# Kernel tuning notes

Hardware: AMD Instinct MI355X
Metric: run time of the kernel (lower is better)

The kernel has to match this reference:

```python
import jax, jax.numpy as jnp
import numpy as np

PAD = 0
EPS = 1e-5


def setup_inputs() -> dict:
    key = jax.random.key(0)
    k1, k2, k3, k4, k5 = jax.random.split(key, 5)
    B, S, D, H = 16, 1024, 512, 4
    output = jax.random.normal(k1, (B, S, D), dtype=jnp.float32)
    local_cor = jax.random.normal(k2, (1,), dtype=jnp.float32)
    event_type = jax.random.randint(k3, (B, S), 0, 1000, dtype=jnp.int64)
    # xavier-ish scale for the per-layer Linear weights
    W = jax.random.normal(k4, (H, D, D), dtype=jnp.float32) * (1.0 / np.sqrt(D))
    b = jax.random.normal(k5, (H, D), dtype=jnp.float32) * 0.01
    return {"output": output, "local_cor": local_cor, "event_type": event_type, "W": W, "b": b}


def _build_mask(event_type, S, dtype):
    # subsequent mask: 1 for strictly-future positions (triu, diag=1)
    subseq = jnp.triu(jnp.ones((S, S), dtype=dtype), k=1)  # [S,S]
    # key-pad mask: 1 where key token is PAD, broadcast over query dim
    keypad = (event_type == PAD).astype(dtype)[:, None, :]  # [B,1,S]
    return ((keypad + subseq[None]) > 0).astype(dtype)  # [B,S,S]


def reference(output, local_cor, event_type, W, b):
    B, S, D = output.shape
    H = W.shape[0]
    temperature = jnp.asarray(D, output.dtype) ** 0.5
    mask = _build_mask(event_type, S, output.dtype)  # [B,S,S]

    x = output
    total = None
    for h in range(H):  # heads are applied SEQUENTIALLY in the original
        # masked QK^T scores
        attn = jnp.einsum('bqd,bkd->bqk', x / temperature, x) * mask  # [B,S,S]
        # L2 normalize along keys (F.normalize p=2, eps=1e-5)
        norm = jnp.sqrt(jnp.sum(attn * attn, axis=-1, keepdims=True))
        attn = attn / jnp.maximum(norm, EPS)
        # value path: ELU(Linear(x))
        v = jax.nn.elu(jnp.einsum('bsd,ed->bse', x, W[h]) + b[h])  # [B,S,D]
        x = jnp.einsum('bqk,bkd->bqd', attn, v)
        total = x if total is None else total + x
    return total
```

## Files before the change

kernel.cpp:

```cpp
#include <hip/hip_runtime.h>
#include <math.h>

#define B_ 16
#define S_ 1024
#define D_ 512
#define H_ 4
#define INV_TEMP 0.044194173824159216f
#define C_SCALE 0.00390625f
#define OUT_SCALE 256.0f

typedef _Float16 f16;
typedef _Float16 f16x8 __attribute__((ext_vector_type(8)));
typedef _Float16 f16x4 __attribute__((ext_vector_type(4)));
typedef float f32x4 __attribute__((ext_vector_type(4)));

#define AS1(p) ((const __attribute__((address_space(1))) void*)(p))
#define AS3(p) ((__attribute__((address_space(3))) void*)(p))
#define MFMA __builtin_amdgcn_mfma_f32_16x16x32_f16

#define SBAR()                                                                 \
    do {                                                                       \
        __builtin_amdgcn_sched_barrier(0);                                     \
        __builtin_amdgcn_s_barrier();                                          \
        __builtin_amdgcn_sched_barrier(0);                                     \
    } while (0)
#define VMF(N)                                                                 \
    do {                                                                       \
        __builtin_amdgcn_sched_barrier(0);                                     \
        asm volatile("s_waitcnt vmcnt(" #N ")" ::: "memory");                  \
        __builtin_amdgcn_sched_barrier(0);                                     \
    } while (0)

__device__ __forceinline__ f16x8 ds_rd16(unsigned addr)
{
    f16x8 r;
    asm volatile("ds_read_b128 %0, %1" : "=v"(r) : "v"(addr));
    return r;
}

__global__ __launch_bounds__(256)
void k_pre(const float* __restrict__ x0, f16* __restrict__ xh,
           const float* __restrict__ W, f16* __restrict__ Wh,
           const int* __restrict__ etype, int* __restrict__ flag,
           float* __restrict__ ssb)
{
    const int t = threadIdx.x;
    const int bi = blockIdx.x;
    if (bi < 8192) {
        const int xcd = bi & 7, j = bi >> 3;
        const int b = 2 * xcd + (j & 1);
        const int off = j >> 1;
        const int i = (b * 512 + off) * 256 + t;
        const float4 v = ((const float4*)x0)[i];
        f16x4 h; h[0] = (f16)v.x; h[1] = (f16)v.y; h[2] = (f16)v.z; h[3] = (f16)v.w;
        ((f16x4*)xh)[i] = h;
    } else if (bi < 9216) {
        const int i = (bi - 8192) * 256 + t;
        const float4 v = ((const float4*)W)[i];
        f16x4 h; h[0] = (f16)v.x; h[1] = (f16)v.y; h[2] = (f16)v.z; h[3] = (f16)v.w;
        ((f16x4*)Wh)[i] = h;
    } else if (bi == 9216) {
        if (t < 128) {
            const int b = t >> 3, kt = t & 7;
            const int* p = etype + b * S_ + kt * 128;
            int any0 = 0;
#pragma unroll
            for (int i = 0; i < 128; i += 4) {
                const int4 v = *(const int4*)(p + i);
                any0 |= (v.x == 0) | (v.y == 0) | (v.z == 0) | (v.w == 0);
            }
            flag[t] = any0;
        }
    } else {
        const int i = (bi - 9217) * 256 + t;
        ((float4*)ssb)[i] = make_float4(0.f, 0.f, 0.f, 0.f);
    }
}

__device__ __forceinline__ void stage128x64(const f16* __restrict__ src, int ld,
                                            char* lds0, int t)
{
    const int r = t >> 3;
    const int c = ((t & 7) ^ (r & 7)) << 3;
    const f16* g = src + (size_t)r * ld + c;
#pragma unroll
    for (int j = 0; j < 4; ++j)
        __builtin_amdgcn_global_load_lds(AS1(g + (size_t)(32 * j) * ld),
                                         AS3(lds0 + j * 4096 + t * 16), 16, 0, 0);
}

__device__ __forceinline__ void mma_asm(unsigned aB, unsigned bB,
                                        const unsigned (*offA)[2],
                                        const unsigned (*offB)[2],
                                        f32x4 (*acc)[4])
{
    f16x8 af[4][2], bf[4][2];
#pragma unroll
    for (int kk = 0; kk < 2; ++kk) {
#pragma unroll
        for (int i = 0; i < 4; ++i) af[i][kk] = ds_rd16(aB + offA[i][kk]);
#pragma unroll
        for (int j = 0; j < 4; ++j) bf[j][kk] = ds_rd16(bB + offB[j][kk]);
    }
    asm volatile("s_waitcnt lgkmcnt(0)" ::: "memory");
    __builtin_amdgcn_sched_barrier(0);
#pragma unroll
    for (int kk = 0; kk < 2; ++kk)
#pragma unroll
        for (int i = 0; i < 4; ++i)
#pragma unroll
            for (int j = 0; j < 4; ++j)
                acc[i][j] = MFMA(af[i][kk], bf[j][kk], acc[i][j], 0, 0, 0);
}

__device__ __forceinline__ void gemm_cnt(const f16* __restrict__ A, int ldA,
                                         const f16* __restrict__ Bm, int ldB,
                                         char* lds, int t,
                                         const unsigned (*offA)[2],
                                         const unsigned (*offB)[2],
                                         f32x4 (*acc)[4])
{
    const unsigned base = (unsigned)(unsigned long long)AS3(lds);
    stage128x64(A, ldA, lds, t);
    stage128x64(Bm, ldB, lds + 16384, t);
#pragma unroll 1
    for (int i = 0; i < 3; ++i) {
        const int k1 = i * 128 + 64, k2 = i * 128 + 128;
        stage128x64(A + k1, ldA, lds + 32768, t);
        stage128x64(Bm + k1, ldB, lds + 49152, t);
        VMF(8); SBAR();
        mma_asm(base, base + 16384, offA, offB, acc);
        SBAR();
        stage128x64(A + k2, ldA, lds, t);
        stage128x64(Bm + k2, ldB, lds + 16384, t);
        VMF(8); SBAR();
        mma_asm(base + 32768, base + 49152, offA, offB, acc);
        SBAR();
    }
    stage128x64(A + 448, ldA, lds + 32768, t);
    stage128x64(Bm + 448, ldB, lds + 49152, t);
    VMF(8); SBAR();
    mma_asm(base, base + 16384, offA, offB, acc);
    SBAR();
    VMF(0); SBAR();
    mma_asm(base + 32768, base + 49152, offA, offB, acc);
}

__global__ __launch_bounds__(256)
void k_vs(const f16* __restrict__ xh, const f16* __restrict__ Wh,
          const float* __restrict__ bias, f16* __restrict__ vT,
          const int* __restrict__ etype, const int* __restrict__ flag,
          f16* __restrict__ sh, float* __restrict__ ss)
{
    __shared__ __align__(16) char lds[65536];
    const int t = threadIdx.x;
    const int w = t >> 6, lane = t & 63, lr = lane & 15, quad = lane >> 4;
    const int wm = w & 1, wn = w >> 1;

    unsigned offA[4][2], offB[4][2];
#pragma unroll
    for (int i = 0; i < 4; ++i) {
        const int ra = wm * 64 + i * 16 + lr;
        const int rb = wn * 64 + i * 16 + lr;
#pragma unroll
        for (int kk = 0; kk < 2; ++kk) {
            offA[i][kk] = (unsigned)((ra << 7) + ((((kk << 2) + quad) ^ (ra & 7)) << 4));
            offB[i][kk] = (unsigned)((rb << 7) + ((((kk << 2) + quad) ^ (rb & 7)) << 4));
        }
    }

    if (blockIdx.x < 1024) {
        const int i0 = blockIdx.x;
        const int xcd = i0 & 7, j0 = i0 >> 3;
        const int b = 2 * xcd + (j0 & 1);
        const int tile = j0 >> 1;
        const int bk = (tile & 7) * 128;
        const int bq = (tile >> 3) * 128;
        if (bk < bq && !flag[b * 8 + (bk >> 7)]) return;

        const f16* xb = xh + (size_t)b * S_ * D_;
        f32x4 acc[4][4] = {};
        gemm_cnt(xb + (size_t)bk * D_, D_, xb + (size_t)bq * D_, D_,
                 lds, t, offA, offB, acc);
        const float sc = INV_TEMP * C_SCALE;
        float ssq[4] = {0.0f, 0.0f, 0.0f, 0.0f};
#pragma unroll
        for (int i = 0; i < 4; ++i) {
            const int k4 = bk + wm * 64 + i * 16 + quad * 4;
            const int4 et = *(const int4*)(etype + b * S_ + k4);
            const int ev[4] = {et.x, et.y, et.z, et.w};
#pragma unroll
            for (int j = 0; j < 4; ++j) {
                const int q = bq + wn * 64 + j * 16 + lr;
                f16x4 hv;
#pragma unroll
                for (int r = 0; r < 4; ++r) {
                    const bool keep = ((k4 + r) > q) || (ev[r] == 0);
                    hv[r] = (f16)(keep ? acc[i][j][r] * sc : 0.0f);
                    const float fv = (float)hv[r];
                    ssq[j] += fv * fv;
                }
                *(f16x4*)(sh + ((size_t)b * S_ + q) * S_ + k4) = hv;
            }
        }
#pragma unroll
        for (int j = 0; j < 4; ++j) {
            float v = ssq[j];
            v += __shfl_xor(v, 16, 64);
            v += __shfl_xor(v, 32, 64);
            if (quad == 0) {
                const int q = bq + wn * 64 + j * 16 + lr;
                atomicAdd(ss + b * S_ + q, v);
            }
        }
    } else {
        const int idx = blockIdx.x - 1024;
        const int xcd = idx & 7;
        const int b = 2 * xcd + ((idx >> 3) & 1);
        const int rest = idx >> 4;
        const int sq = rest & 7;
        const int bn = (rest >> 3) * 128;
        const int bm = b * 1024 + sq * 128;
        f32x4 acc[4][4] = {};
        gemm_cnt(xh + (size_t)bm * D_, D_, Wh + (size_t)bn * D_, D_,
                 lds, t, offA, offB, acc);
#pragma unroll
        for (int j = 0; j < 4; ++j) {
            const int e = bn + wn * 64 + j * 16 + lr;
            const float be = bias[e];
#pragma unroll
            for (int i = 0; i < 4; ++i) {
                const int s = sq * 128 + wm * 64 + i * 16 + quad * 4;
                f16x4 hv;
#pragma unroll
                for (int r = 0; r < 4; ++r) {
                    float z = acc[i][j][r] + be;
                    z = (z > 0.0f) ? z : (expf(z) - 1.0f);
                    hv[r] = (f16)z;
                }
                *(f16x4*)(vT + ((size_t)b * D_ + e) * S_ + s) = hv;
            }
        }
    }
}

__device__ __forceinline__ void mma64(const char* ldsA, const char* ldsB,
                                      int wm, int wn, int lr, int quad,
                                      f32x4 (*acc)[4])
{
#pragma unroll
    for (int kk = 0; kk < 2; ++kk) {
        f16x8 af[4], bf[4];
#pragma unroll
        for (int i = 0; i < 4; ++i) {
            const int row = wm * 64 + i * 16 + lr;
            af[i] = *(const f16x8*)(ldsA + (row << 7) +
                                    ((((kk << 2) + quad) ^ (row & 7)) << 4));
        }
#pragma unroll
        for (int j = 0; j < 4; ++j) {
            const int row = wn * 64 + j * 16 + lr;
            bf[j] = *(const f16x8*)(ldsB + (row << 7) +
                                    ((((kk << 2) + quad) ^ (row & 7)) << 4));
        }
#pragma unroll
        for (int i = 0; i < 4; ++i)
#pragma unroll
            for (int j = 0; j < 4; ++j)
                acc[i][j] = MFMA(af[i], bf[j], acc[i][j], 0, 0, 0);
    }
}

__global__ __launch_bounds__(512)
void k_out(const f16* __restrict__ vT, const f16* __restrict__ sh,
           const float* __restrict__ ss, const int* __restrict__ flag,
           f16* __restrict__ xh_w,
           const f16* __restrict__ xs0, const f16* __restrict__ xs1,
           const f16* __restrict__ xs2,
           float* __restrict__ out, const int accum, const int wout)
{
    __shared__ __align__(16) char lds[65536];
    __shared__ int klist[32];
    __shared__ int kcnt;
    const int t = threadIdx.x;
    const int g = t >> 8;
    const int tl = t & 255;
    const int w = tl >> 6, lane = tl & 63, lr = lane & 15, quad = lane >> 4;
    const int wm = w & 1, wn = w >> 1;
    const int i0 = blockIdx.x;
    const int xcd = i0 & 7, j0 = i0 >> 3;
    const int b = 2 * xcd + (j0 & 1);
    const int tile = j0 >> 1;
    const int be = (tile & 3) * 128;
    const int bq = (tile >> 2) * 128;
    const int qt = bq >> 7;

    if (t == 0) {
        int n = 0;
        for (int kc = 0; kc < 8; ++kc)
            if (kc >= qt || flag[b * 8 + kc]) {
                const int kb = kc * 128;
                klist[n] = kb; klist[n + 1] = kb + 32;
                klist[n + 2] = kb + 64; klist[n + 3] = kb + 96;
                n += 4;
            }
        kcnt = n;
    }
    __syncthreads();
    const int half = kcnt >> 1;
    const int s0 = g ? half : 0;

    const f16* Abase = vT + ((size_t)b * D_ + be) * S_;
    const f16* Bbase = sh + ((size_t)b * S_ + bq) * S_;
    char* myl = lds + (g << 15);
    f32x4 acc[4][4] = {};
#pragma unroll 1
    for (int i = 0; i < half; i += 2) {
        const int k0 = klist[s0 + i];
        stage128x64(Abase + k0, S_, myl, tl);
        stage128x64(Bbase + k0, S_, myl + 16384, tl);
        __syncthreads();
        mma64(myl, myl + 16384, wm, wn, lr, quad, acc);
        __syncthreads();
    }

    if (g == 1) {
#pragma unroll
        for (int j = 0; j < 4; ++j)
#pragma unroll
            for (int i = 0; i < 4; ++i)
                *(f32x4*)(lds + (((w * 16 + j * 4 + i) * 64 + lane) << 4)) = acc[i][j];
    }
    __syncthreads();
    if (g == 0) {
#pragma unroll
        for (int j = 0; j < 4; ++j) {
            const int q = bq + wn * 64 + j * 16 + lr;
            const float ssv = ss[b * S_ + q];
            const float scl = 1.0f / (C_SCALE * fmaxf(sqrtf(ssv) * OUT_SCALE, 1e-5f));
#pragma unroll
            for (int i = 0; i < 4; ++i) {
                const f32x4 other =
                    *(const f32x4*)(lds + (((w * 16 + j * 4 + i) * 64 + lane) << 4));
                const f32x4 sum = acc[i][j] + other;
                const int e4 = be + wm * 64 + i * 16 + quad * 4;
                const size_t o = ((size_t)b * S_ + q) * D_ + e4;
                f32x4 val;
                f16x4 hx;
#pragma unroll
                for (int r = 0; r < 4; ++r) {
                    val[r] = sum[r] * scl;
                    hx[r] = (f16)val[r];
                }
                if (xh_w) *(f16x4*)(xh_w + o) = hx;
                if (xs0) {
                    const f16x4 a0 = *(const f16x4*)(xs0 + o);
                    const f16x4 a1 = *(const f16x4*)(xs1 + o);
                    const f16x4 a2 = *(const f16x4*)(xs2 + o);
#pragma unroll
                    for (int r = 0; r < 4; ++r)
                        val[r] += (float)a0[r] + (float)a1[r] + (float)a2[r];
                }
                if (wout) {
                    f32x4 v2 = val;
                    if (accum) { const f32x4 old = *(const f32x4*)(out + o); v2 = v2 + old; }
                    *(f32x4*)(out + o) = v2;
                }
            }
        }
    }
}

extern "C" void kernel_launch(void* const* d_in, const int* in_sizes, int n_in,
                              void* d_out, int out_size, void* d_ws, size_t ws_size,
                              hipStream_t stream) {
    const float* x0    = (const float*)d_in[0];
    const int*   etype = (const int*)d_in[2];
    const float* W     = (const float*)d_in[3];
    const float* bias  = (const float*)d_in[4];
    float* out = (float*)d_out;

    char* ws = (char*)d_ws;
    f16*   xA    = (f16*)(ws);
    f16*   vT    = (f16*)(ws + (16u << 20));
    f16*   sh    = (f16*)(ws + (32u << 20));
    f16*   Wh    = (f16*)(ws + (64u << 20));
    float* ssb   = (float*)(ws + (66u << 20));
    int*   flags = (int*)(ws + (66u << 20) + 262144);

    const bool big = ws_size >= ((size_t)101 << 20);
    f16* xB = big ? (f16*)(ws + (68u << 20)) : xA;
    f16* xC = big ? (f16*)(ws + (84u << 20)) : xA;

    k_pre<<<9281, 256, 0, stream>>>(x0, xA, W, Wh, etype, flags, ssb);

    f16* xin[H_]  = {xA, xA, xB, xC};
    f16* xdst[H_] = {xA, xB, xC, nullptr};

    for (int h = 0; h < H_; ++h) {
        float* ss = ssb + (size_t)h * B_ * S_;
        k_vs <<<1536, 256, 0, stream>>>(xin[h], Wh + (size_t)h * D_ * D_,
                                        bias + (size_t)h * D_, vT,
                                        etype, flags, sh, ss);
        if (big) {
            const bool last = (h == H_ - 1);
            k_out<<<512, 512, 0, stream>>>(vT, sh, ss, flags, xdst[h],
                                           last ? xA : nullptr,
                                           last ? xB : nullptr,
                                           last ? xC : nullptr,
                                           out, 0, last ? 1 : 0);
        } else {
            k_out<<<512, 512, 0, stream>>>(vT, sh, ss, flags,
                                           (h < H_ - 1) ? xA : nullptr,
                                           nullptr, nullptr, nullptr,
                                           out, h > 0, 1);
        }
    }
}
```

Measured before the change: 323.4 us.

## Replace split-K two-group k_out with double-buffered single-group pipeline

k_out drops its two 256-thread groups that each covered half of the K range and then reduced through LDS. It now runs one 256-thread block that double-buffers 64-wide K tiles in LDS, issuing the next tile's async loads while MFMA (via an asm helper with precomputed swizzled offsets) consumes the current one. This removes the LDS partial-sum reduction and overlaps global loads with compute. The cost is half as many threads per block, so less parallelism within each tile's K loop.

```diff
diff --git a/kernel.cpp b/kernel.cpp
--- a/kernel.cpp
+++ b/kernel.cpp
@@ -244,34 +244,7 @@
     }
 }
 
-__device__ __forceinline__ void mma64(const char* ldsA, const char* ldsB,
-                                      int wm, int wn, int lr, int quad,
-                                      f32x4 (*acc)[4])
-{
-#pragma unroll
-    for (int kk = 0; kk < 2; ++kk) {
-        f16x8 af[4], bf[4];
-#pragma unroll
-        for (int i = 0; i < 4; ++i) {
-            const int row = wm * 64 + i * 16 + lr;
-            af[i] = *(const f16x8*)(ldsA + (row << 7) +
-                                    ((((kk << 2) + quad) ^ (row & 7)) << 4));
-        }
-#pragma unroll
-        for (int j = 0; j < 4; ++j) {
-            const int row = wn * 64 + j * 16 + lr;
-            bf[j] = *(const f16x8*)(ldsB + (row << 7) +
-                                    ((((kk << 2) + quad) ^ (row & 7)) << 4));
-        }
-#pragma unroll
-        for (int i = 0; i < 4; ++i)
-#pragma unroll
-            for (int j = 0; j < 4; ++j)
-                acc[i][j] = MFMA(af[i], bf[j], acc[i][j], 0, 0, 0);
-    }
-}
-
-__global__ __launch_bounds__(512)
+__global__ __launch_bounds__(256)
 void k_out(const f16* __restrict__ vT, const f16* __restrict__ sh,
            const float* __restrict__ ss, const int* __restrict__ flag,
            f16* __restrict__ xh_w,
@@ -280,12 +253,10 @@
            float* __restrict__ out, const int accum, const int wout)
 {
     __shared__ __align__(16) char lds[65536];
-    __shared__ int klist[32];
-    __shared__ int kcnt;
+    __shared__ int k64[16];
+    __shared__ int nsteps;
     const int t = threadIdx.x;
-    const int g = t >> 8;
-    const int tl = t & 255;
-    const int w = tl >> 6, lane = tl & 63, lr = lane & 15, quad = lane >> 4;
+    const int w = t >> 6, lane = t & 63, lr = lane & 15, quad = lane >> 4;
     const int wm = w & 1, wn = w >> 1;
     const int i0 = blockIdx.x;
     const int xcd = i0 & 7, j0 = i0 >> 3;
@@ -299,73 +270,92 @@
         int n = 0;
         for (int kc = 0; kc < 8; ++kc)
             if (kc >= qt || flag[b * 8 + kc]) {
-                const int kb = kc * 128;
-                klist[n] = kb; klist[n + 1] = kb + 32;
-                klist[n + 2] = kb + 64; klist[n + 3] = kb + 96;
-                n += 4;
-            }
-        kcnt = n;
+                k64[n]     = kc * 128;
+                k64[n + 1] = kc * 128 + 64;
+                n += 2;
+            }
+        nsteps = n;
     }
     __syncthreads();
-    const int half = kcnt >> 1;
-    const int s0 = g ? half : 0;
-
+    const int ns = nsteps;
+
+    unsigned offA[4][2], offB[4][2];
+#pragma unroll
+    for (int i = 0; i < 4; ++i) {
+        const int ra = wm * 64 + i * 16 + lr;
+        const int rb = wn * 64 + i * 16 + lr;
+#pragma unroll
+        for (int kk = 0; kk < 2; ++kk) {
+            offA[i][kk] = (unsigned)((ra << 7) + ((((kk << 2) + quad) ^ (ra & 7)) << 4));
+            offB[i][kk] = (unsigned)((rb << 7) + ((((kk << 2) + quad) ^ (rb & 7)) << 4));
+        }
+    }
+
+    const unsigned base = (unsigned)(unsigned long long)AS3(lds);
     const f16* Abase = vT + ((size_t)b * D_ + be) * S_;
     const f16* Bbase = sh + ((size_t)b * S_ + bq) * S_;
-    char* myl = lds + (g << 15);
     f32x4 acc[4][4] = {};
+
+    stage128x64(Abase + k64[0], S_, lds, t);
+    stage128x64(Bbase + k64[0], S_, lds + 16384, t);
+    int i = 1;
 #pragma unroll 1
-    for (int i = 0; i < half; i += 2) {
-        const int k0 = klist[s0 + i];
-        stage128x64(Abase + k0, S_, myl, tl);
-        stage128x64(Bbase + k0, S_, myl + 16384, tl);
-        __syncthreads();
-        mma64(myl, myl + 16384, wm, wn, lr, quad, acc);
-        __syncthreads();
-    }
-
-    if (g == 1) {
-#pragma unroll
-        for (int j = 0; j < 4; ++j)
-#pragma unroll
-            for (int i = 0; i < 4; ++i)
-                *(f32x4*)(lds + (((w * 16 + j * 4 + i) * 64 + lane) << 4)) = acc[i][j];
-    }
-    __syncthreads();
-    if (g == 0) {
-#pragma unroll
-        for (int j = 0; j < 4; ++j) {
-            const int q = bq + wn * 64 + j * 16 + lr;
-            const float ssv = ss[b * S_ + q];
-            const float scl = 1.0f / (C_SCALE * fmaxf(sqrtf(ssv) * OUT_SCALE, 1e-5f));
-#pragma unroll
-            for (int i = 0; i < 4; ++i) {
-                const f32x4 other =
-                    *(const f32x4*)(lds + (((w * 16 + j * 4 + i) * 64 + lane) << 4));
-                const f32x4 sum = acc[i][j] + other;
-                const int e4 = be + wm * 64 + i * 16 + quad * 4;
-                const size_t o = ((size_t)b * S_ + q) * D_ + e4;
-                f32x4 val;
-                f16x4 hx;
-#pragma unroll
-                for (int r = 0; r < 4; ++r) {
-                    val[r] = sum[r] * scl;
-                    hx[r] = (f16)val[r];
-                }
-                if (xh_w) *(f16x4*)(xh_w + o) = hx;
-                if (xs0) {
-                    const f16x4 a0 = *(const f16x4*)(xs0 + o);
-                    const f16x4 a1 = *(const f16x4*)(xs1 + o);
-                    const f16x4 a2 = *(const f16x4*)(xs2 + o);
-#pragma unroll
-                    for (int r = 0; r < 4; ++r)
-                        val[r] += (float)a0[r] + (float)a1[r] + (float)a2[r];
-                }
-                if (wout) {
-                    f32x4 v2 = val;
-                    if (accum) { const f32x4 old = *(const f32x4*)(out + o); v2 = v2 + old; }
-                    *(f32x4*)(out + o) = v2;
-                }
+    for (; i + 1 < ns; i += 2) {
+        const int ka = k64[i], kb = k64[i + 1];
+        stage128x64(Abase + ka, S_, lds + 32768, t);
+        stage128x64(Bbase + ka, S_, lds + 49152, t);
+        VMF(8); SBAR();
+        mma_asm(base, base + 16384, offA, offB, acc);
+        SBAR();
+        stage128x64(Abase + kb, S_, lds, t);
+        stage128x64(Bbase + kb, S_, lds + 16384, t);
+        VMF(8); SBAR();
+        mma_asm(base + 32768, base + 49152, offA, offB, acc);
+        SBAR();
+    }
+    if (i < ns) {
+        const int ka = k64[i];
+        stage128x64(Abase + ka, S_, lds + 32768, t);
+        stage128x64(Bbase + ka, S_, lds + 49152, t);
+        VMF(8); SBAR();
+        mma_asm(base, base + 16384, offA, offB, acc);
+        SBAR();
+        VMF(0); SBAR();
+        mma_asm(base + 32768, base + 49152, offA, offB, acc);
+    } else {
+        VMF(0); SBAR();
+        mma_asm(base, base + 16384, offA, offB, acc);
+    }
+
+#pragma unroll
+    for (int j = 0; j < 4; ++j) {
+        const int q = bq + wn * 64 + j * 16 + lr;
+        const float ssv = ss[b * S_ + q];
+        const float scl = 1.0f / (C_SCALE * fmaxf(sqrtf(ssv) * OUT_SCALE, 1e-5f));
+#pragma unroll
+        for (int i2 = 0; i2 < 4; ++i2) {
+            const int e4 = be + wm * 64 + i2 * 16 + quad * 4;
+            const size_t o = ((size_t)b * S_ + q) * D_ + e4;
+            f32x4 val;
+            f16x4 hx;
+#pragma unroll
+            for (int r = 0; r < 4; ++r) {
+                val[r] = acc[i2][j][r] * scl;
+                hx[r] = (f16)val[r];
+            }
+            if (xh_w) *(f16x4*)(xh_w + o) = hx;
+            if (xs0) {
+                const f16x4 a0 = *(const f16x4*)(xs0 + o);
+                const f16x4 a1 = *(const f16x4*)(xs1 + o);
+                const f16x4 a2 = *(const f16x4*)(xs2 + o);
+#pragma unroll
+                for (int r = 0; r < 4; ++r)
+                    val[r] += (float)a0[r] + (float)a1[r] + (float)a2[r];
+            }
+            if (wout) {
+                f32x4 v2 = val;
+                if (accum) { const f32x4 old = *(const f32x4*)(out + o); v2 = v2 + old; }
+                *(f32x4*)(out + o) = v2;
             }
         }
     }
@@ -404,13 +394,13 @@
                                         etype, flags, sh, ss);
         if (big) {
             const bool last = (h == H_ - 1);
-            k_out<<<512, 512, 0, stream>>>(vT, sh, ss, flags, xdst[h],
+            k_out<<<512, 256, 0, stream>>>(vT, sh, ss, flags, xdst[h],
                                            last ? xA : nullptr,
                                            last ? xB : nullptr,
                                            last ? xC : nullptr,
                                            out, 0, last ? 1 : 0);
         } else {
-            k_out<<<512, 512, 0, stream>>>(vT, sh, ss, flags,
+            k_out<<<512, 256, 0, stream>>>(vT, sh, ss, flags,
                                            (h < H_ - 1) ? xA : nullptr,
                                            nullptr, nullptr, nullptr,
                                            out, h > 0, 1);
```

Result: slower. 333.9 us (+3.3%).
